# Optimization experiments

Hardware: AMD Instinct MI355X
Metric: run time of the kernel (lower is better)

## Reference

```python
import jax, jax.numpy as jnp
import numpy as np

Q_DIM, KV_DIM, H = 64, 64, 4


def setup_inputs() -> dict:
    key = jax.random.key(0)
    ks = jax.random.split(key, 8)
    b, t = 8, 128
    q_x = jax.random.normal(ks[0], (b, t, Q_DIM), dtype=jnp.float32)
    kv_x = jax.random.normal(ks[1], (b, t, t - 1, KV_DIM), dtype=jnp.float32)
    # nn.Linear weights: (out_features, in_features), applied as x @ W.T
    Wk = jax.random.normal(ks[2], (KV_DIM * H, KV_DIM), dtype=jnp.float32) * 0.05
    Wq = jax.random.normal(ks[3], (KV_DIM * H, Q_DIM), dtype=jnp.float32) * 0.05
    Wv = jax.random.normal(ks[4], (KV_DIM * H, KV_DIM), dtype=jnp.float32) * 0.05
    bias = jax.random.uniform(ks[5], (KV_DIM,), minval=-0.1, maxval=0.1, dtype=jnp.float32)
    Ws = jax.random.normal(ks[6], (1, KV_DIM), dtype=jnp.float32) * 0.05
    bs = jax.random.normal(ks[7], (1,), dtype=jnp.float32) * 0.05
    return {"q_x": q_x, "kv_x": kv_x, "Wk": Wk, "Wq": Wq, "Wv": Wv,
            "bias": bias, "Ws": Ws, "bs": bs}


def reference(q_x, kv_x, Wk, Wq, Wv, bias, Ws, bs):
    b, t, tm1, k = kv_x.shape  # tm1 == t-1
    h = H
    # keys: (b, t, t-1, h, k)
    keys = (kv_x @ Wk.T).reshape(b, t, tm1, h, k)
    # queries: (b, t, 1, h, k)
    queries = (q_x @ Wq.T).reshape(b, t, 1, h, k)
    # additive tanh score projected to scalar per (b,t,n,h)
    act = jnp.tanh(keys + queries + bias)
    score = jnp.einsum('btnhk,k->btnh', act, Ws[0]) + bs[0]
    # softmax over the t-1 key axis (dim=2)
    w = jax.nn.softmax(score, axis=2)  # (b, t, t-1, h)
    values = (kv_x @ Wv.T).reshape(b, t, tm1, h, k)
    # weighted sum over t-1
    x = jnp.einsum('btnh,btnhk->bthk', w, values)
    return x.reshape(b, t, h * k)
```

## Files before the change

### kernel.cpp

```cpp
#include <hip/hip_runtime.h>
#include <math.h>

#define B 8
#define T 128
#define NKEY 127
#define KDIM 64
#define NH 4
#define CH 256

typedef _Float16 half8 __attribute__((ext_vector_type(8)));
typedef float floatx4 __attribute__((ext_vector_type(4)));

__device__ __forceinline__ float fast_tanh(float x) {
    float e = __expf(2.f * x);
    float r = __builtin_amdgcn_rcpf(e + 1.f);
    return fmaf(-2.f, r, 1.f);
}

__device__ __forceinline__ half8 cvt8(const float4& a, const float4& b) {
    half8 h;
    h[0] = (_Float16)a.x; h[1] = (_Float16)a.y;
    h[2] = (_Float16)a.z; h[3] = (_Float16)a.w;
    h[4] = (_Float16)b.x; h[5] = (_Float16)b.y;
    h[6] = (_Float16)b.z; h[7] = (_Float16)b.w;
    return h;
}

__global__ __launch_bounds__(256, 4)
void attn_kernel(const float* __restrict__ q_x,
                 const float* __restrict__ kv_x,
                 const float* __restrict__ Wk,
                 const float* __restrict__ Wq,
                 const float* __restrict__ Wv,
                 const float* __restrict__ bias,
                 const float* __restrict__ Ws,
                 const float* __restrict__ bs,
                 float* __restrict__ out)
{
    __shared__ __align__(16) _Float16 bh_lds[16][64][8];
    __shared__ __align__(16) float qb_lds[128];
    __shared__ __align__(16) float pp_lds[4][128];

    float* const probs = (float*)bh_lds;
    float* const wkv2  = (float*)bh_lds + 256;

    const int bt   = blockIdx.x & 1023;
    const int hp   = blockIdx.x >> 10;
    const int tid  = threadIdx.x;
    const int wid  = tid >> 6;
    const int lane = tid & 63;
    const int col  = lane & 15;
    const int quad = lane >> 4;
    const int h2   = wid & 1;
    const int role = wid >> 1;
    const int hg   = hp * 2 + h2;

    const float* __restrict__ kvg = kv_x + (size_t)bt * NKEY * KDIM;

    #pragma unroll
    for (int w = 0; w < 4; ++w) {
        const int chunk = w * 4 + wid;
        const int nt = chunk >> 1, ks = chunk & 1;
        const int n  = nt * 16 + col;
        const int k0 = ks * 32 + quad * 8;
        float4 a = make_float4(0.f, 0.f, 0.f, 0.f);
        float4 b = make_float4(0.f, 0.f, 0.f, 0.f);
        if (n < NKEY) {
            const float* p = kvg + (size_t)n * KDIM + k0;
            a = *(const float4*)p;
            b = *(const float4*)(p + 4);
        }
        *(half8*)&bh_lds[chunk][lane][0] = cvt8(a, b);
    }

    half8 ah[2][2];
    #pragma unroll
    for (int jtl = 0; jtl < 2; ++jtl)
        #pragma unroll
        for (int ks = 0; ks < 2; ++ks) {
            const float* wrow = Wk + (size_t)(hg * 64 + role * 32 + jtl * 16 + col) * KDIM
                                   + ks * 32 + quad * 8;
            float4 a = *(const float4*)wrow;
            float4 b = *(const float4*)(wrow + 4);
            ah[jtl][ks] = cvt8(a, b);
        }

    {
        const int c = tid >> 1, kh = tid & 1;
        const float4* Wq4 = (const float4*)(Wq + (size_t)(hp * 128 + c) * KDIM + kh * 32);
        const float4* q4g = (const float4*)(q_x + (size_t)bt * KDIM + kh * 32);
        float4 qa = make_float4(0.f, 0.f, 0.f, 0.f);
        #pragma unroll
        for (int i = 0; i < 8; ++i) {
            float4 w = Wq4[i];
            float4 q4 = q4g[i];
            qa.x = fmaf(q4.x, w.x, qa.x);
            qa.y = fmaf(q4.y, w.y, qa.y);
            qa.z = fmaf(q4.z, w.z, qa.z);
            qa.w = fmaf(q4.w, w.w, qa.w);
        }
        float r = (qa.x + qa.y) + (qa.z + qa.w);
        r += __shfl_xor(r, 1, 64);
        if (kh == 0) qb_lds[c] = r + bias[c & 63];
    }

    __syncthreads();

    floatx4 qb4[2];
    float4  wsv[2];
    #pragma unroll
    for (int jtl = 0; jtl < 2; ++jtl) {
        qb4[jtl] = *(const floatx4*)&qb_lds[h2 * 64 + role * 32 + jtl * 16 + quad * 4];
        wsv[jtl] = *(const float4*)&Ws[role * 32 + jtl * 16 + quad * 4];
    }

    #pragma unroll
    for (int nt = 0; nt < 8; ++nt) {
        half8 b0 = *(const half8*)&bh_lds[nt * 2 + 0][lane][0];
        half8 b1 = *(const half8*)&bh_lds[nt * 2 + 1][lane][0];
        float partial = 0.f;
        #pragma unroll
        for (int jtl = 0; jtl < 2; ++jtl) {
            floatx4 c = qb4[jtl];
            c = __builtin_amdgcn_mfma_f32_16x16x32_f16(ah[jtl][0], b0, c, 0, 0, 0);
            c = __builtin_amdgcn_mfma_f32_16x16x32_f16(ah[jtl][1], b1, c, 0, 0, 0);
            #pragma unroll
            for (int r = 0; r < 4; ++r)
                partial = fmaf(fast_tanh(c[r]), wsv[jtl][r], partial);
        }
        partial += __shfl_xor(partial, 16, 64);
        partial += __shfl_xor(partial, 32, 64);
        if (lane < 16) pp_lds[wid][nt * 16 + lane] = partial;
    }

    __syncthreads();

    float invl;
    {
        float s_a = pp_lds[h2][lane]      + pp_lds[2 + h2][lane];
        float s_b = pp_lds[h2][64 + lane] + pp_lds[2 + h2][64 + lane];
        if (lane == 63) s_b = -1e30f;
        float mx = fmaxf(s_a, s_b);
        #pragma unroll
        for (int off = 32; off > 0; off >>= 1)
            mx = fmaxf(mx, __shfl_xor(mx, off, 64));
        float pa = __expf(s_a - mx);
        float pb = __expf(s_b - mx);
        float ls = pa + pb;
        #pragma unroll
        for (int off = 32; off > 0; off >>= 1)
            ls += __shfl_xor(ls, off, 64);
        invl = 1.f / ls;
        if (role == 0) {
            probs[h2 * 128 + lane]      = pa;
            probs[h2 * 128 + 64 + lane] = pb;
        }
    }

    __syncthreads();

    {
        const float* kvl = kvg + lane;
        const float* pr  = probs + h2 * 128;
        const int n0 = role * 64;
        float w0 = 0.f, w1 = 0.f, w2 = 0.f, w3 = 0.f;
        #pragma unroll 4
        for (int n4 = n0; n4 < n0 + 64; n4 += 4) {
            float4 p4 = *(const float4*)&pr[n4];
            const int n3 = (n4 + 3 < NKEY) ? (n4 + 3) : 0;
            w0 = fmaf(p4.x, kvl[(size_t)(n4 + 0) * KDIM], w0);
            w1 = fmaf(p4.y, kvl[(size_t)(n4 + 1) * KDIM], w1);
            w2 = fmaf(p4.z, kvl[(size_t)(n4 + 2) * KDIM], w2);
            w3 = fmaf(p4.w, kvl[(size_t)n3 * KDIM], w3);
        }
        wkv2[wid * 64 + lane] = ((w0 + w1) + (w2 + w3)) * invl;
    }

    __syncthreads();

    {
        const int c = tid >> 1, kh = tid & 1;
        const int hc = c >> 6;
        const float4* wa  = (const float4*)&wkv2[hc * 64 + kh * 32];
        const float4* wb  = (const float4*)&wkv2[(2 + hc) * 64 + kh * 32];
        const float4* Wv4 = (const float4*)(Wv + (size_t)(hp * 128 + c) * KDIM + kh * 32);
        float4 oa = make_float4(0.f, 0.f, 0.f, 0.f);
        #pragma unroll
        for (int i = 0; i < 8; ++i) {
            float4 w = Wv4[i];
            float4 v = wa[i];
            float4 u = wb[i];
            oa.x = fmaf(v.x + u.x, w.x, oa.x);
            oa.y = fmaf(v.y + u.y, w.y, oa.y);
            oa.z = fmaf(v.z + u.z, w.z, oa.z);
            oa.w = fmaf(v.w + u.w, w.w, oa.w);
        }
        float r = (oa.x + oa.y) + (oa.z + oa.w);
        r += __shfl_xor(r, 1, 64);
        if (kh == 0) out[(size_t)bt * CH + hp * 128 + c] = r;
    }
}

extern "C" void kernel_launch(void* const* d_in, const int* in_sizes, int n_in,
                              void* d_out, int out_size, void* d_ws, size_t ws_size,
                              hipStream_t stream) {
    const float* q_x  = (const float*)d_in[0];
    const float* kv_x = (const float*)d_in[1];
    const float* Wk   = (const float*)d_in[2];
    const float* Wq   = (const float*)d_in[3];
    const float* Wv   = (const float*)d_in[4];
    const float* bias = (const float*)d_in[5];
    const float* Ws   = (const float*)d_in[6];
    const float* bs   = (const float*)d_in[7];
    float* out = (float*)d_out;

    attn_kernel<<<dim3(2 * B * T), dim3(256), 0, stream>>>(
        q_x, kv_x, Wk, Wq, Wv, bias, Ws, bs, out);
}
```

Measured before the change: 123.6 us.

## Merge head-pair blocks into one 512-thread block per (b,t) row

Each block now processes all four heads for one (b,t) row with eight waves, instead of two blocks each handling two heads. The kv_x tile is converted and staged into LDS once and shared across all heads, halving global reads of kv_x and removing duplicate setup work. The tighter launch bound may restrict registers and reduce scheduling flexibility.

```diff
diff --git a/kernel.cpp b/kernel.cpp
--- a/kernel.cpp
+++ b/kernel.cpp
@@ -26,7 +26,7 @@
     return h;
 }
 
-__global__ __launch_bounds__(256, 4)
+__global__ __launch_bounds__(512, 8)
 void attn_kernel(const float* __restrict__ q_x,
                  const float* __restrict__ kv_x,
                  const float* __restrict__ Wk,
@@ -38,28 +38,26 @@
                  float* __restrict__ out)
 {
     __shared__ __align__(16) _Float16 bh_lds[16][64][8];
-    __shared__ __align__(16) float qb_lds[128];
-    __shared__ __align__(16) float pp_lds[4][128];
+    __shared__ __align__(16) float qb_lds[CH];
+    __shared__ __align__(16) float pp_lds[8][128];
 
     float* const probs = (float*)bh_lds;
-    float* const wkv2  = (float*)bh_lds + 256;
-
-    const int bt   = blockIdx.x & 1023;
-    const int hp   = blockIdx.x >> 10;
+    float* const wkv2  = (float*)bh_lds + 512;
+
+    const int bt   = blockIdx.x;
     const int tid  = threadIdx.x;
     const int wid  = tid >> 6;
     const int lane = tid & 63;
     const int col  = lane & 15;
     const int quad = lane >> 4;
-    const int h2   = wid & 1;
-    const int role = wid >> 1;
-    const int hg   = hp * 2 + h2;
+    const int h    = wid & 3;
+    const int role = wid >> 2;
 
     const float* __restrict__ kvg = kv_x + (size_t)bt * NKEY * KDIM;
 
     #pragma unroll
-    for (int w = 0; w < 4; ++w) {
-        const int chunk = w * 4 + wid;
+    for (int w = 0; w < 2; ++w) {
+        const int chunk = w * 8 + wid;
         const int nt = chunk >> 1, ks = chunk & 1;
         const int n  = nt * 16 + col;
         const int k0 = ks * 32 + quad * 8;
@@ -78,7 +76,7 @@
     for (int jtl = 0; jtl < 2; ++jtl)
         #pragma unroll
         for (int ks = 0; ks < 2; ++ks) {
-            const float* wrow = Wk + (size_t)(hg * 64 + role * 32 + jtl * 16 + col) * KDIM
+            const float* wrow = Wk + (size_t)(h * 64 + role * 32 + jtl * 16 + col) * KDIM
                                    + ks * 32 + quad * 8;
             float4 a = *(const float4*)wrow;
             float4 b = *(const float4*)(wrow + 4);
@@ -87,7 +85,7 @@
 
     {
         const int c = tid >> 1, kh = tid & 1;
-        const float4* Wq4 = (const float4*)(Wq + (size_t)(hp * 128 + c) * KDIM + kh * 32);
+        const float4* Wq4 = (const float4*)(Wq + (size_t)c * KDIM + kh * 32);
         const float4* q4g = (const float4*)(q_x + (size_t)bt * KDIM + kh * 32);
         float4 qa = make_float4(0.f, 0.f, 0.f, 0.f);
         #pragma unroll
@@ -110,7 +108,7 @@
     float4  wsv[2];
     #pragma unroll
     for (int jtl = 0; jtl < 2; ++jtl) {
-        qb4[jtl] = *(const floatx4*)&qb_lds[h2 * 64 + role * 32 + jtl * 16 + quad * 4];
+        qb4[jtl] = *(const floatx4*)&qb_lds[h * 64 + role * 32 + jtl * 16 + quad * 4];
         wsv[jtl] = *(const float4*)&Ws[role * 32 + jtl * 16 + quad * 4];
     }
 
@@ -137,8 +135,8 @@
 
     float invl;
     {
-        float s_a = pp_lds[h2][lane]      + pp_lds[2 + h2][lane];
-        float s_b = pp_lds[h2][64 + lane] + pp_lds[2 + h2][64 + lane];
+        float s_a = pp_lds[h][lane]      + pp_lds[4 + h][lane];
+        float s_b = pp_lds[h][64 + lane] + pp_lds[4 + h][64 + lane];
         if (lane == 63) s_b = -1e30f;
         float mx = fmaxf(s_a, s_b);
         #pragma unroll
@@ -152,8 +150,8 @@
             ls += __shfl_xor(ls, off, 64);
         invl = 1.f / ls;
         if (role == 0) {
-            probs[h2 * 128 + lane]      = pa;
-            probs[h2 * 128 + 64 + lane] = pb;
+            probs[h * 128 + lane]      = pa;
+            probs[h * 128 + 64 + lane] = pb;
         }
     }
 
@@ -161,7 +159,7 @@
 
     {
         const float* kvl = kvg + lane;
-        const float* pr  = probs + h2 * 128;
+        const float* pr  = probs + h * 128;
         const int n0 = role * 64;
         float w0 = 0.f, w1 = 0.f, w2 = 0.f, w3 = 0.f;
         #pragma unroll 4
@@ -182,8 +180,8 @@
         const int c = tid >> 1, kh = tid & 1;
         const int hc = c >> 6;
         const float4* wa  = (const float4*)&wkv2[hc * 64 + kh * 32];
-        const float4* wb  = (const float4*)&wkv2[(2 + hc) * 64 + kh * 32];
-        const float4* Wv4 = (const float4*)(Wv + (size_t)(hp * 128 + c) * KDIM + kh * 32);
+        const float4* wb  = (const float4*)&wkv2[(4 + hc) * 64 + kh * 32];
+        const float4* Wv4 = (const float4*)(Wv + (size_t)c * KDIM + kh * 32);
         float4 oa = make_float4(0.f, 0.f, 0.f, 0.f);
         #pragma unroll
         for (int i = 0; i < 8; ++i) {
@@ -197,7 +195,7 @@
         }
         float r = (oa.x + oa.y) + (oa.z + oa.w);
         r += __shfl_xor(r, 1, 64);
-        if (kh == 0) out[(size_t)bt * CH + hp * 128 + c] = r;
+        if (kh == 0) out[(size_t)bt * CH + c] = r;
     }
 }
 
@@ -214,6 +212,6 @@
     const float* bs   = (const float*)d_in[7];
     float* out = (float*)d_out;
 
-    attn_kernel<<<dim3(2 * B * T), dim3(256), 0, stream>>>(
+    attn_kernel<<<dim3(B * T), dim3(512), 0, stream>>>(
         q_x, kv_x, Wk, Wq, Wv, bias, Ws, bs, out);
 }
```

Result: no change. 123.1 us (-0.4%).
